# Kernel tuning notes

Hardware: AMD Instinct MI355X
Metric: run time of the kernel (lower is better)

Reference implementation:

```python
import jax, jax.numpy as jnp
import numpy as np

B, S, D, H = 2, 2048, 1024, 16
DK = D // H  # d_query_key_output = d_head = 64


def setup_inputs() -> dict:
    key = jax.random.key(0)
    ks = jax.random.split(key, 16)
    p = 0.02
    return {
        "input_q": jax.random.normal(ks[0], (B, S, D), jnp.float32),
        "input_k": jax.random.normal(ks[1], (B, S, D), jnp.float32),
        "input_v": jax.random.normal(ks[2], (B, S, D), jnp.float32),
        "mask": jax.random.randint(ks[3], (B, 1, S, S), 0, 2, jnp.int32),
        "attention_propagation": jax.random.normal(ks[4], (S, S), jnp.float32) * p,
        "Wq": jax.random.normal(ks[5], (D, H * DK), jnp.float32) * p,
        "bq": jnp.zeros((H * DK,), jnp.float32),
        "Wk": jax.random.normal(ks[6], (D, H * DK), jnp.float32) * p,
        "bk": jnp.zeros((H * DK,), jnp.float32),
        "Wv": jax.random.normal(ks[7], (D, H * DK), jnp.float32) * p,
        "bv": jnp.zeros((H * DK,), jnp.float32),
        "Wo": jax.random.normal(ks[8], (H * DK, D), jnp.float32) * p,
        "bo": jnp.zeros((D,), jnp.float32),
    }


def reference(input_q, input_k, input_v, mask, attention_propagation,
              Wq, bq, Wk, bk, Wv, bv, Wo, bo):
    b, q_len, _ = input_q.shape
    kv_len = input_k.shape[-2]
    # project and split into heads: split(d, -1) + stack(-3) == reshape + transpose
    q = (input_q @ Wq + bq).reshape(b, q_len, H, DK).transpose(0, 2, 1, 3)   # [B,H,Q,dk]
    k = (input_k @ Wk + bk).reshape(b, kv_len, H, DK).transpose(0, 2, 1, 3)  # [B,H,K,dk]
    v = (input_v @ Wv + bv).reshape(b, kv_len, H, DK).transpose(0, 2, 1, 3)  # [B,H,K,dh]

    scale = jnp.sqrt(jnp.asarray(DK, dtype=q.dtype))
    qk = jnp.einsum('bhqd,bhkd->bhqk', q, k) / scale                         # [B,H,Q,K]

    m = mask.astype(bool)  # [B,1,Q,K], broadcasts over heads
    # attention propagation branch: zero masked scores, then scores @ prop^T
    aw = jnp.where(m, qk, jnp.asarray(0.0, qk.dtype))
    aw = jnp.einsum('bhqk,lk->bhql', aw, attention_propagation)
    # masked softmax with nan_to_num for fully-masked rows
    aw = jnp.where(m, aw, -jnp.inf)
    aw = jax.nn.softmax(aw, axis=-1)
    aw = jnp.nan_to_num(aw, nan=0.0)
    # dropout is identity in eval / dropout_rate=0
    out = jnp.einsum('bhqk,bhkd->bhqd', aw, v)                               # [B,H,Q,dh]
    out = out.transpose(0, 2, 1, 3).reshape(b, q_len, H * DK)                # concat heads
    return out @ Wo + bo
```

## Files before the change

kernel.cpp:

```cpp
#include <hip/hip_runtime.h>
#include <hip/hip_bf16.h>
#include <stdint.h>

typedef unsigned int u32;
typedef __attribute__((ext_vector_type(8))) short bf16x8;
typedef __attribute__((ext_vector_type(4))) float f32x4;
typedef __attribute__((ext_vector_type(16))) float f32x16;

#define MFMA16(a, b, c) __builtin_amdgcn_mfma_f32_16x16x32_bf16((a), (b), (c), 0, 0, 0)
#define MFMA32(a, b, c) __builtin_amdgcn_mfma_f32_32x32x16_bf16((a), (b), (c), 0, 0, 0)

__device__ __forceinline__ float bf2f(short s) {
    union { u32 u; float f; } v;
    v.u = ((u32)(unsigned short)s) << 16;
    return v.f;
}
__device__ __forceinline__ short f2bf(float f) {
    union { float f; u32 u; } v; v.f = f;
    u32 r = (v.u + 0x7fffu + ((v.u >> 16) & 1u)) >> 16;
    return (short)r;
}
__device__ __forceinline__ void gl_lds16(const short* g, short* l) {
    __builtin_amdgcn_global_load_lds(
        (const __attribute__((address_space(1))) u32*)g,
        (__attribute__((address_space(3))) u32*)l, 16, 0, 0);
}

__device__ __forceinline__ void stage_tile(const short* g, int ld, short* lds) {
    int wave = threadIdx.x >> 6, lane = threadIdx.x & 63;
#pragma unroll
    for (int i = 0; i < 4; ++i) {
        int r0 = i * 32 + wave * 8;
        int r  = r0 + (lane >> 3);
        int c8 = (lane & 7) ^ (r & 7);
        gl_lds16(g + (long)r * ld + c8 * 8, lds + r0 * 64);
    }
}
__device__ __forceinline__ bf16x8 frag64(const short* lds, int row, int k8) {
    return *(const bf16x8*)(lds + row * 64 + ((k8 ^ (row & 7)) * 8));
}

__device__ __forceinline__ void stage_tile_p(const short* g, int ld, short* lds) {
    int wave = threadIdx.x >> 6, lane = threadIdx.x & 63;
#pragma unroll
    for (int i = 0; i < 4; ++i) {
        int r0 = i * 32 + wave * 8;
        int r  = r0 + (lane >> 3);
        int c8 = (lane & 7) ^ (r & 7);
        gl_lds16(g + (long)r * ld + c8 * 8, lds + r0 * 64 + (r0 >> 3) * 8);
    }
}
__device__ __forceinline__ bf16x8 frag64p(const short* lds, int row, int k8) {
    return *(const bf16x8*)(lds + row * 64 + ((row >> 3) * 8) + ((k8 ^ (row & 7)) * 8));
}

__global__ __launch_bounds__(256) void probe_dtype(const short* __restrict__ x,
                                                   int* __restrict__ flag) {
    __shared__ int cnt;
    if (threadIdx.x == 0) cnt = 0;
    __syncthreads();
    int c = 0;
    for (int i = threadIdx.x; i < 2048; i += 256) {
        int e = ((int)(unsigned short)x[i] >> 7) & 0xFF;
        if (e >= 147) ++c;
    }
    atomicAdd(&cnt, c);
    __syncthreads();
    if (threadIdx.x == 0) flag[0] = (cnt > 100) ? 1 : 0;
}

__global__ __launch_bounds__(256) void pack_mask(const int* __restrict__ mask,
                                                 u32* __restrict__ mb) {
    int row = blockIdx.x * 4 + (threadIdx.x >> 6);
    int lane = threadIdx.x & 63;
    const int* src = mask + (long)row * 2048;
    u32* dst = mb + (long)row * 64;
    for (int c0 = 0; c0 < 2048; c0 += 64) {
        unsigned long long m = __ballot(src[c0 + lane] != 0);
        if (lane == 0) {
            dst[(c0 >> 5)]     = (u32)m;
            dst[(c0 >> 5) + 1] = (u32)(m >> 32);
        }
    }
}
__device__ __forceinline__ int mask_bit(const u32* mb, int b, int row, int col) {
    u32 w = mb[((long)b * 2048 + row) * 64 + (col >> 5)];
    return (w >> (col & 31)) & 1;
}

__global__ __launch_bounds__(256) void convert_bf16(const void* __restrict__ src,
                                                    short* __restrict__ dst, int n,
                                                    const int* __restrict__ flag) {
    int isf = flag[0];
    for (int i = blockIdx.x * 256 + threadIdx.x; i < n; i += gridDim.x * 256)
        dst[i] = isf ? f2bf(((const float*)src)[i]) : ((const short*)src)[i];
}

__global__ __launch_bounds__(256) void convert_biases(const void* s0, const void* s1,
                                                      const void* s2, const void* s3,
                                                      short* __restrict__ dst,
                                                      const int* __restrict__ flag) {
    const void* ss[4] = { s0, s1, s2, s3 };
    const void* s = ss[blockIdx.x];
    short* d = dst + blockIdx.x * 1024;
    int isf = flag[0];
    for (int i = threadIdx.x; i < 1024; i += 256)
        d[i] = isf ? f2bf(((const float*)s)[i]) : ((const short*)s)[i];
}

__global__ __launch_bounds__(256) void transpose_1024(const void* __restrict__ src,
                                                      short* __restrict__ dst,
                                                      const int* __restrict__ flag) {
    __shared__ short t[64][65];
    int isf = flag[0];
    int r0 = blockIdx.y * 64, c0 = blockIdx.x * 64;
    int tx = threadIdx.x & 63, ty = threadIdx.x >> 6;
#pragma unroll
    for (int i = 0; i < 16; ++i) {
        int r = ty + i * 4;
        long idx = (long)(r0 + r) * 1024 + c0 + tx;
        t[r][tx] = isf ? f2bf(((const float*)src)[idx]) : ((const short*)src)[idx];
    }
    __syncthreads();
#pragma unroll
    for (int i = 0; i < 16; ++i) {
        int r = ty + i * 4;
        dst[(long)(c0 + r) * 1024 + r0 + tx] = t[tx][r];
    }
}

__global__ __launch_bounds__(256) void build_vt(const short* __restrict__ vp,
                                                short* __restrict__ vt) {
    __shared__ short t[64][65];
    int bh = blockIdx.y, b = bh >> 4, h = bh & 15;
    int l0 = blockIdx.x * 64;
    int tx = threadIdx.x & 63, ty = threadIdx.x >> 6;
#pragma unroll
    for (int i = 0; i < 16; ++i) {
        int l = ty + i * 4;
        t[l][tx] = vp[((long)b * 2048 + l0 + l) * 1024 + h * 64 + tx];
    }
    __syncthreads();
#pragma unroll
    for (int i = 0; i < 16; ++i) {
        int d = ty + i * 4;
        vt[((long)bh * 80 + d) * 2048 + l0 + tx] = t[tx][d];
    }
#pragma unroll
    for (int dd = 0; dd < 4; ++dd) {
        int d = 64 + ty * 4 + dd;
        short v = (d == 64) ? f2bf(1.0f) : (short)0;
        vt[((long)bh * 80 + d) * 2048 + l0 + tx] = v;
    }
}

__global__ __launch_bounds__(256) void gemm_nt_bias(const short* __restrict__ A,
                                                    const short* __restrict__ Bt,
                                                    const short* __restrict__ bias,
                                                    void* __restrict__ C,
                                                    int K, int lda, int ldb, int ldc,
                                                    const int* __restrict__ outf32) {
    __shared__ __align__(16) short a_lds[128 * 64];
    __shared__ __align__(16) short b_lds[128 * 64];
    int m0 = blockIdx.y * 128, n0 = blockIdx.x * 128;
    int wave = threadIdx.x >> 6, lane = threadIdx.x & 63;
    int col = lane & 15, quad = lane >> 4;
    int wm = (wave >> 1) * 64, wn = (wave & 1) * 64;
    f32x4 acc[4][4] = {};
    for (int k0 = 0; k0 < K; k0 += 64) {
        stage_tile(A + (long)m0 * lda + k0, lda, a_lds);
        stage_tile(Bt + (long)n0 * ldb + k0, ldb, b_lds);
        __syncthreads();
#pragma unroll
        for (int ks = 0; ks < 2; ++ks) {
            bf16x8 af[4], bfr[4];
#pragma unroll
            for (int t = 0; t < 4; ++t) af[t]  = frag64(a_lds, wm + t * 16 + col, ks * 4 + quad);
#pragma unroll
            for (int t = 0; t < 4; ++t) bfr[t] = frag64(b_lds, wn + t * 16 + col, ks * 4 + quad);
#pragma unroll
            for (int mt = 0; mt < 4; ++mt)
#pragma unroll
                for (int nt = 0; nt < 4; ++nt)
                    acc[mt][nt] = MFMA16(af[mt], bfr[nt], acc[mt][nt]);
        }
        __syncthreads();
    }
    int of = outf32 ? outf32[0] : 0;
#pragma unroll
    for (int mt = 0; mt < 4; ++mt) {
        int rb = m0 + wm + mt * 16 + quad * 4;
#pragma unroll
        for (int nt = 0; nt < 4; ++nt) {
            int c = n0 + wn + nt * 16 + col;
            float bv = bf2f(bias[c]);
#pragma unroll
            for (int r = 0; r < 4; ++r) {
                float v = acc[mt][nt][r] + bv;
                if (!(v == v)) v = 0.0f;
                long idx = (long)(rb + r) * ldc + c;
                if (of) ((float*)C)[idx] = v;
                else    ((short*)C)[idx] = f2bf(v);
            }
        }
    }
}

__global__ __launch_bounds__(256) void qk_mask_gemm(const short* __restrict__ qp,
                                                    const short* __restrict__ kp,
                                                    const u32* __restrict__ mb,
                                                    short* __restrict__ Smat,
                                                    int h0) {
    __shared__ __align__(16) short a_lds[128 * 64];
    __shared__ __align__(16) short b_lds[128 * 64];
    int zl = blockIdx.z, bh = h0 + zl, b = bh >> 4, h = bh & 15;
    int m0 = blockIdx.y * 128, n0 = blockIdx.x * 128;
    int wave = threadIdx.x >> 6, lane = threadIdx.x & 63;
    int col = lane & 15, quad = lane >> 4;
    int wm = (wave >> 1) * 64, wn = (wave & 1) * 64;
    const short* Aq = qp + ((long)b * 2048 + m0) * 1024 + h * 64;
    const short* Bk = kp + ((long)b * 2048 + n0) * 1024 + h * 64;
    stage_tile(Aq, 1024, a_lds);
    stage_tile(Bk, 1024, b_lds);
    __syncthreads();
    f32x4 acc[4][4] = {};
#pragma unroll
    for (int ks = 0; ks < 2; ++ks) {
        bf16x8 af[4], bfr[4];
#pragma unroll
        for (int t = 0; t < 4; ++t) af[t]  = frag64(a_lds, wm + t * 16 + col, ks * 4 + quad);
#pragma unroll
        for (int t = 0; t < 4; ++t) bfr[t] = frag64(b_lds, wn + t * 16 + col, ks * 4 + quad);
#pragma unroll
        for (int mt = 0; mt < 4; ++mt)
#pragma unroll
            for (int nt = 0; nt < 4; ++nt)
                acc[mt][nt] = MFMA16(af[mt], bfr[nt], acc[mt][nt]);
    }
#pragma unroll
    for (int mt = 0; mt < 4; ++mt) {
        int qb = m0 + wm + mt * 16 + quad * 4;
#pragma unroll
        for (int nt = 0; nt < 4; ++nt) {
            int kg = n0 + wn + nt * 16 + col;
#pragma unroll
            for (int r = 0; r < 4; ++r) {
                int qg = qb + r;
                int mk = mask_bit(mb, b, qg, kg);
                float v = mk ? acc[mt][nt][r] * 0.125f : 0.0f;
                if (!(v == v)) v = 0.0f;
                Smat[((long)zl * 2048 + qg) * 2048 + kg] = f2bf(v);
            }
        }
    }
}

__global__ __launch_bounds__(256) void p_gemm_exp(const short* __restrict__ Smat,
                                                  const short* __restrict__ prop,
                                                  const u32* __restrict__ mb,
                                                  short* __restrict__ Pmat,
                                                  int h0) {
    __shared__ __align__(16) short a_lds[128 * 64 + 128];
    __shared__ __align__(16) short b_lds[128 * 64 + 128];
    int zl = blockIdx.z, bh = h0 + zl, b = bh >> 4;
    int m0 = blockIdx.y * 128, n0 = blockIdx.x * 128;
    int wave = threadIdx.x >> 6, lane = threadIdx.x & 63;
    int m32 = lane & 31, hi = lane >> 5;
    int wm = (wave >> 1) * 64, wn = (wave & 1) * 64;
    const short* Arow = Smat + ((long)zl * 2048 + m0) * 2048;
    f32x16 acc[2][2] = {};
    for (int k0 = 0; k0 < 2048; k0 += 64) {
        stage_tile_p(Arow + k0, 2048, a_lds);
        stage_tile_p(prop + (long)n0 * 2048 + k0, 2048, b_lds);
        __syncthreads();
#pragma unroll
        for (int kc = 0; kc < 4; ++kc) {
            int k8 = kc * 2 + hi;
            bf16x8 af[2], bfr[2];
#pragma unroll
            for (int t = 0; t < 2; ++t) af[t]  = frag64p(a_lds, wm + t * 32 + m32, k8);
#pragma unroll
            for (int t = 0; t < 2; ++t) bfr[t] = frag64p(b_lds, wn + t * 32 + m32, k8);
#pragma unroll
            for (int mt = 0; mt < 2; ++mt)
#pragma unroll
                for (int nt = 0; nt < 2; ++nt)
                    acc[mt][nt] = MFMA32(af[mt], bfr[nt], acc[mt][nt]);
        }
        __syncthreads();
    }
#pragma unroll
    for (int mt = 0; mt < 2; ++mt) {
#pragma unroll
        for (int nt = 0; nt < 2; ++nt) {
            int lg = n0 + wn + nt * 32 + m32;
#pragma unroll
            for (int reg = 0; reg < 16; ++reg) {
                int qg = m0 + wm + mt * 32 + (reg & 3) + 8 * (reg >> 2) + 4 * hi;
                int mk = mask_bit(mb, b, qg, lg);
                float pv = acc[mt][nt][reg];
                if (!(pv == pv)) pv = 0.0f;
                pv = fminf(pv, 30.0f);
                float e = mk ? __expf(pv) : 0.0f;
                Pmat[((long)zl * 2048 + qg) * 2048 + lg] = f2bf(e);
            }
        }
    }
}

__global__ __launch_bounds__(256) void pv_kernel(const short* __restrict__ Pmat,
                                                 const short* __restrict__ vt,
                                                 short* __restrict__ att,
                                                 int h0) {
    __shared__ __align__(16) short p_lds[128 * 128];
    __shared__ __align__(16) short v_lds[80 * 128];
    int bhl = blockIdx.y, bh = h0 + bhl, b = bh >> 4, h = bh & 15;
    int q0 = blockIdx.x * 128;
    int wave = threadIdx.x >> 6, lane = threadIdx.x & 63;
    int col = lane & 15, quad = lane >> 4;
    const short* Pbase = Pmat + ((long)bhl * 2048 + q0) * 2048;
    const short* vbase = vt + (long)bh * 80 * 2048;

    f32x4 oacc[2][5] = {};

    for (int lt = 0; lt < 16; ++lt) {
        int l0 = lt * 128;
#pragma unroll
        for (int i = 0; i < 8; ++i) {
            int r0 = i * 16 + wave * 4;
            int r  = r0 + (lane >> 4);
            int c16 = (lane & 15) ^ (r & 15);
            gl_lds16(Pbase + (long)r * 2048 + l0 + c16 * 8, p_lds + r0 * 128);
        }
#pragma unroll
        for (int i = 0; i < 5; ++i) {
            int r0 = (wave * 5 + i) * 4;
            int r  = r0 + (lane >> 4);
            int c16 = (lane & 15) ^ (r & 15);
            gl_lds16(vbase + (long)r * 2048 + l0 + c16 * 8, v_lds + r0 * 128);
        }
        __syncthreads();
#pragma unroll
        for (int ks = 0; ks < 4; ++ks) {
            bf16x8 paf[2], vbf[5];
            int k8 = ks * 4 + quad;
#pragma unroll
            for (int t = 0; t < 2; ++t) {
                int rr = wave * 32 + t * 16 + col;
                paf[t] = *(const bf16x8*)(p_lds + rr * 128 + ((k8 ^ (rr & 15)) * 8));
            }
#pragma unroll
            for (int t = 0; t < 5; ++t) {
                int d = t * 16 + col;
                vbf[t] = *(const bf16x8*)(v_lds + d * 128 + ((k8 ^ (d & 15)) * 8));
            }
#pragma unroll
            for (int mt = 0; mt < 2; ++mt)
#pragma unroll
                for (int nt = 0; nt < 5; ++nt)
                    oacc[mt][nt] = MFMA16(paf[mt], vbf[nt], oacc[mt][nt]);
        }
        __syncthreads();
    }
#pragma unroll
    for (int mt = 0; mt < 2; ++mt) {
#pragma unroll
        for (int r = 0; r < 4; ++r) {
            float denom = __shfl(oacc[mt][4][r], lane & 48, 64);
            float inv = (denom > 1e-20f) ? 1.0f / denom : 0.0f;
            int qrow = q0 + wave * 32 + mt * 16 + quad * 4 + r;
#pragma unroll
            for (int nt = 0; nt < 4; ++nt) {
                float v = oacc[mt][nt][r] * inv;
                if (!(v == v)) v = 0.0f;
                att[((long)b * 2048 + qrow) * 1024 + h * 64 + nt * 16 + col] = f2bf(v);
            }
        }
    }
}

__global__ __launch_bounds__(256) void attn_fused(const short* __restrict__ Smat,
                                                  const short* __restrict__ prop,
                                                  const short* __restrict__ vt,
                                                  const u32* __restrict__ mb,
                                                  short* __restrict__ att,
                                                  int h0) {
    __shared__ __align__(16) short ab_lds[2 * 128 * 64];
    __shared__ __align__(16) short v_lds[80 * 128];
    short* p_lds = ab_lds;
    int bhl = blockIdx.y, bh = h0 + bhl, b = bh >> 4, h = bh & 15;
    int q0 = blockIdx.x * 128;
    int wave = threadIdx.x >> 6, lane = threadIdx.x & 63;
    int col = lane & 15, quad = lane >> 4;
    int wm = (wave >> 1) * 64, wn = (wave & 1) * 64;
    const short* Arow = Smat + ((long)bhl * 2048 + q0) * 2048;
    const short* vbase = vt + (long)bh * 80 * 2048;
    {
        u32* z1 = (u32*)ab_lds;
        u32* z2 = (u32*)v_lds;
        for (int i = threadIdx.x; i < 8192; i += 256) z1[i] = 0;
        for (int i = threadIdx.x; i < 5120; i += 256) z2[i] = 0;
    }
    __syncthreads();
    f32x4 oacc[2][5] = {};
    for (int lt = 0; lt < 16; ++lt) {
        int l0 = lt * 128;
#pragma unroll
        for (int i = 0; i < 5; ++i) {
            int r0 = (wave * 5 + i) * 4;
            int r  = r0 + (lane >> 4);
            int c16 = (lane & 15) ^ (r & 15);
            gl_lds16(vbase + (long)r * 2048 + l0 + c16 * 8, v_lds + r0 * 128);
        }
        f32x4 pacc[4][4] = {};
        for (int k0 = 0; k0 < 2048; k0 += 64) {
            stage_tile(Arow + k0, 2048, ab_lds);
            stage_tile(prop + (long)l0 * 2048 + k0, 2048, ab_lds + 128 * 64);
            __syncthreads();
#pragma unroll
            for (int ks = 0; ks < 2; ++ks) {
                bf16x8 af[4], bfr[4];
#pragma unroll
                for (int t = 0; t < 4; ++t) af[t]  = frag64(ab_lds, wm + t * 16 + col, ks * 4 + quad);
#pragma unroll
                for (int t = 0; t < 4; ++t) bfr[t] = frag64(ab_lds + 128 * 64, wn + t * 16 + col, ks * 4 + quad);
#pragma unroll
                for (int mt = 0; mt < 4; ++mt)
#pragma unroll
                    for (int nt = 0; nt < 4; ++nt)
                        pacc[mt][nt] = MFMA16(af[mt], bfr[nt], pacc[mt][nt]);
            }
            __syncthreads();
        }
#pragma unroll
        for (int mt = 0; mt < 4; ++mt) {
            int rm = wm + mt * 16 + quad * 4;
#pragma unroll
            for (int nt = 0; nt < 4; ++nt) {
                int cl = wn + nt * 16 + col;
                int lg = l0 + cl;
                int k8 = cl >> 3;
#pragma unroll
                for (int r = 0; r < 4; ++r) {
                    int rr = rm + r;
                    int mk = mask_bit(mb, b, q0 + rr, lg);
                    float pv = pacc[mt][nt][r];
                    if (!(pv == pv)) pv = 0.0f;
                    pv = fminf(pv, 30.0f);
                    float e = mk ? __expf(pv) : 0.0f;
                    p_lds[rr * 128 + ((k8 ^ (rr & 15)) * 8) + (cl & 7)] = f2bf(e);
                }
            }
        }
        __syncthreads();
#pragma unroll
        for (int ks = 0; ks < 4; ++ks) {
            bf16x8 paf[2], vbf[5];
            int k8 = ks * 4 + quad;
#pragma unroll
            for (int t = 0; t < 2; ++t) {
                int rr = wave * 32 + t * 16 + col;
                paf[t] = *(const bf16x8*)(p_lds + rr * 128 + ((k8 ^ (rr & 15)) * 8));
            }
#pragma unroll
            for (int t = 0; t < 5; ++t) {
                int d = t * 16 + col;
                vbf[t] = *(const bf16x8*)(v_lds + d * 128 + ((k8 ^ (d & 15)) * 8));
            }
#pragma unroll
            for (int mt = 0; mt < 2; ++mt)
#pragma unroll
                for (int nt = 0; nt < 5; ++nt)
                    oacc[mt][nt] = MFMA16(paf[mt], vbf[nt], oacc[mt][nt]);
        }
        __syncthreads();
    }
#pragma unroll
    for (int mt = 0; mt < 2; ++mt) {
#pragma unroll
        for (int r = 0; r < 4; ++r) {
            float denom = __shfl(oacc[mt][4][r], lane & 48, 64);
            float inv = (denom > 1e-20f) ? 1.0f / denom : 0.0f;
            int qrow = q0 + wave * 32 + mt * 16 + quad * 4 + r;
#pragma unroll
            for (int nt = 0; nt < 4; ++nt) {
                float v = oacc[mt][nt][r] * inv;
                if (!(v == v)) v = 0.0f;
                att[((long)b * 2048 + qrow) * 1024 + h * 64 + nt * 16 + col] = f2bf(v);
            }
        }
    }
}

extern "C" void kernel_launch(void* const* d_in, const int* in_sizes, int n_in,
                              void* d_out, int out_size, void* d_ws, size_t ws_size,
                              hipStream_t stream) {
    const void* xq   = d_in[0];
    const void* xk   = d_in[1];
    const void* xv   = d_in[2];
    const int*  mask = (const int*)d_in[3];
    const void* prop = d_in[4];
    const void* Wq   = d_in[5];
    const void* bq   = d_in[6];
    const void* Wk   = d_in[7];
    const void* bk   = d_in[8];
    const void* Wv   = d_in[9];
    const void* bv   = d_in[10];
    const void* Wo   = d_in[11];
    const void* bo   = d_in[12];

    char* ws = (char*)d_ws;
    const size_t MB = 1ull << 20;
    short* qp   = (short*)(ws + 0 * MB);
    short* kp   = (short*)(ws + 8 * MB);
    short* vp   = (short*)(ws + 16 * MB);
    short* attb = (short*)(ws + 24 * MB);
    short* WqT  = (short*)(ws + 32 * MB);
    short* WkT  = (short*)(ws + 34 * MB);
    short* WvT  = (short*)(ws + 36 * MB);
    short* WoT  = (short*)(ws + 38 * MB);
    short* vtb  = (short*)(ws + 40 * MB);
    u32*   mb   = (u32*)(ws + 50 * MB);
    int*   flag = (int*)(ws + 51 * MB);
    short* bq_c = (short*)(ws + 51 * MB + 4096);
    short* bk_c = bq_c + 1024;
    short* bv_c = bk_c + 1024;
    short* bo_c = bv_c + 1024;

    long wsMB = (long)(ws_size / MB);
    dim3 blk(256);
    const int NTOK = 4096 * 1024;
    const long HEAD_ELEMS = 2048L * 2048;

    if (wsMB < 60) return;

    probe_dtype<<<1, blk, 0, stream>>>((const short*)xq, flag);
    pack_mask<<<1024, blk, 0, stream>>>(mask, mb);
    convert_biases<<<4, blk, 0, stream>>>(bq, bk, bv, bo, bq_c, flag);
    transpose_1024<<<dim3(16, 16), blk, 0, stream>>>(Wq, WqT, flag);
    transpose_1024<<<dim3(16, 16), blk, 0, stream>>>(Wk, WkT, flag);
    transpose_1024<<<dim3(16, 16), blk, 0, stream>>>(Wv, WvT, flag);
    transpose_1024<<<dim3(16, 16), blk, 0, stream>>>(Wo, WoT, flag);

    if (wsMB >= 76) {
        short* prop_c = (short*)(ws + 52 * MB);
        short* xc     = (short*)(ws + 60 * MB);
        short* Smat   = (short*)(ws + 60 * MB);
        int G = (int)((wsMB - 60) / 16);
        if (G > 32) G = 32;
        short* Pmat = Smat + (long)G * HEAD_ELEMS;

        convert_bf16<<<1024, blk, 0, stream>>>(prop, prop_c, NTOK, flag);
        convert_bf16<<<1024, blk, 0, stream>>>(xq, xc, NTOK, flag);
        gemm_nt_bias<<<dim3(8, 32), blk, 0, stream>>>(xc, WqT, bq_c, qp, 1024, 1024, 1024, 1024, nullptr);
        convert_bf16<<<1024, blk, 0, stream>>>(xk, xc, NTOK, flag);
        gemm_nt_bias<<<dim3(8, 32), blk, 0, stream>>>(xc, WkT, bk_c, kp, 1024, 1024, 1024, 1024, nullptr);
        convert_bf16<<<1024, blk, 0, stream>>>(xv, xc, NTOK, flag);
        gemm_nt_bias<<<dim3(8, 32), blk, 0, stream>>>(xc, WvT, bv_c, vp, 1024, 1024, 1024, 1024, nullptr);
        build_vt<<<dim3(32, 32), blk, 0, stream>>>(vp, vtb);

        for (int h0 = 0; h0 < 32; h0 += G) {
            int g = 32 - h0 < G ? 32 - h0 : G;
            qk_mask_gemm<<<dim3(16, 16, g), blk, 0, stream>>>(qp, kp, mb, Smat, h0);
            p_gemm_exp<<<dim3(16, 16, g), blk, 0, stream>>>(Smat, prop_c, mb, Pmat, h0);
            pv_kernel<<<dim3(16, g), blk, 0, stream>>>(Pmat, vtb, attb, h0);
        }
    } else if (wsMB >= 68) {
        short* prop_c = (short*)(ws + 52 * MB);
        short* xc     = (short*)(ws + 60 * MB);
        short* Smat   = (short*)(ws + 60 * MB);
        int G = (int)((wsMB - 60) / 8);
        if (G > 32) G = 32;
        convert_bf16<<<1024, blk, 0, stream>>>(prop, prop_c, NTOK, flag);
        convert_bf16<<<1024, blk, 0, stream>>>(xq, xc, NTOK, flag);
        gemm_nt_bias<<<dim3(8, 32), blk, 0, stream>>>(xc, WqT, bq_c, qp, 1024, 1024, 1024, 1024, nullptr);
        convert_bf16<<<1024, blk, 0, stream>>>(xk, xc, NTOK, flag);
        gemm_nt_bias<<<dim3(8, 32), blk, 0, stream>>>(xc, WkT, bk_c, kp, 1024, 1024, 1024, 1024, nullptr);
        convert_bf16<<<1024, blk, 0, stream>>>(xv, xc, NTOK, flag);
        gemm_nt_bias<<<dim3(8, 32), blk, 0, stream>>>(xc, WvT, bv_c, vp, 1024, 1024, 1024, 1024, nullptr);
        build_vt<<<dim3(32, 32), blk, 0, stream>>>(vp, vtb);
        for (int h0 = 0; h0 < 32; h0 += G) {
            int g = 32 - h0 < G ? 32 - h0 : G;
            qk_mask_gemm<<<dim3(16, 16, g), blk, 0, stream>>>(qp, kp, mb, Smat, h0);
            attn_fused<<<dim3(16, g), blk, 0, stream>>>(Smat, prop_c, vtb, mb, attb, h0);
        }
    } else {
        short* Smat = (short*)(ws + 52 * MB);
        int G = (int)((wsMB - 52) / 8);
        if (G > 32) G = 32;
        gemm_nt_bias<<<dim3(8, 32), blk, 0, stream>>>((const short*)xq, WqT, bq_c, qp, 1024, 1024, 1024, 1024, nullptr);
        gemm_nt_bias<<<dim3(8, 32), blk, 0, stream>>>((const short*)xk, WkT, bk_c, kp, 1024, 1024, 1024, 1024, nullptr);
        gemm_nt_bias<<<dim3(8, 32), blk, 0, stream>>>((const short*)xv, WvT, bv_c, vp, 1024, 1024, 1024, 1024, nullptr);
        build_vt<<<dim3(32, 32), blk, 0, stream>>>(vp, vtb);
        for (int h0 = 0; h0 < 32; h0 += G) {
            int g = 32 - h0 < G ? 32 - h0 : G;
            qk_mask_gemm<<<dim3(16, 16, g), blk, 0, stream>>>(qp, kp, mb, Smat, h0);
            attn_fused<<<dim3(16, g), blk, 0, stream>>>(Smat, (const short*)prop, vtb, mb, attb, h0);
        }
    }

    gemm_nt_bias<<<dim3(8, 32), blk, 0, stream>>>(attb, WoT, bo_c, d_out, 1024, 1024, 1024, 1024, flag);
}
```

Before: 1.157 ms.

## Fuse propagation GEMM with PV product via split-K atomic accumulation

Merges the propagation GEMM + exp kernel with the P·V kernel. Each 128x128 tile of exp-scores stays in LDS, is multiplied by the matching V slice, and is atomically added into an fp32 output buffer. A separate divide kernel then normalises by the accumulated row sum. The softmax denominator now comes from an MFMA against a ones vector instead of a padded ones row in V, which shrinks V^T from 80 to 64 rows. This removes the round trip of the full bf16 P matrix through global memory. In exchange it adds a memset, float atomics, an extra kernel and a reshuffled workspace layout that needs a larger workspace for the fused path.

Result: slower. 1.281 ms (+10.7%).

```diff
diff --git a/kernel.cpp b/kernel.cpp
--- a/kernel.cpp
+++ b/kernel.cpp
@@ -144,13 +144,7 @@
 #pragma unroll
     for (int i = 0; i < 16; ++i) {
         int d = ty + i * 4;
-        vt[((long)bh * 80 + d) * 2048 + l0 + tx] = t[tx][d];
-    }
-#pragma unroll
-    for (int dd = 0; dd < 4; ++dd) {
-        int d = 64 + ty * 4 + dd;
-        short v = (d == 64) ? f2bf(1.0f) : (short)0;
-        vt[((long)bh * 80 + d) * 2048 + l0 + tx] = v;
+        vt[((long)bh * 64 + d) * 2048 + l0 + tx] = t[tx][d];
     }
 }
 
@@ -255,19 +249,33 @@
     }
 }
 
-__global__ __launch_bounds__(256) void p_gemm_exp(const short* __restrict__ Smat,
-                                                  const short* __restrict__ prop,
-                                                  const u32* __restrict__ mb,
-                                                  short* __restrict__ Pmat,
-                                                  int h0) {
-    __shared__ __align__(16) short a_lds[128 * 64 + 128];
-    __shared__ __align__(16) short b_lds[128 * 64 + 128];
+__global__ __launch_bounds__(256) void p_gemm_exp_pv(const short* __restrict__ Smat,
+                                                     const short* __restrict__ prop,
+                                                     const u32* __restrict__ mb,
+                                                     const short* __restrict__ vt,
+                                                     float* __restrict__ Obuf,
+                                                     int h0) {
+    __shared__ __align__(16) short ab_lds[2 * (128 * 64 + 128)];
+    __shared__ __align__(16) short v_lds[64 * 128];
+    short* a_lds = ab_lds;
+    short* b_lds = ab_lds + (128 * 64 + 128);
+    short* p_lds = ab_lds;
     int zl = blockIdx.z, bh = h0 + zl, b = bh >> 4;
     int m0 = blockIdx.y * 128, n0 = blockIdx.x * 128;
     int wave = threadIdx.x >> 6, lane = threadIdx.x & 63;
     int m32 = lane & 31, hi = lane >> 5;
     int wm = (wave >> 1) * 64, wn = (wave & 1) * 64;
     const short* Arow = Smat + ((long)zl * 2048 + m0) * 2048;
+    const short* vbase = vt + (long)bh * 64 * 2048;
+
+#pragma unroll
+    for (int i = 0; i < 4; ++i) {
+        int r0 = (wave * 4 + i) * 4;
+        int r  = r0 + (lane >> 4);
+        int c16 = (lane & 15) ^ (r & 15);
+        gl_lds16(vbase + (long)r * 2048 + n0 + c16 * 8, v_lds + r0 * 128);
+    }
+
     f32x16 acc[2][2] = {};
     for (int k0 = 0; k0 < 2048; k0 += 64) {
         stage_tile_p(Arow + k0, 2048, a_lds);
@@ -289,94 +297,81 @@
         }
         __syncthreads();
     }
+
 #pragma unroll
     for (int mt = 0; mt < 2; ++mt) {
 #pragma unroll
         for (int nt = 0; nt < 2; ++nt) {
-            int lg = n0 + wn + nt * 32 + m32;
+            int cl = wn + nt * 32 + m32;
+            int k8 = cl >> 3;
 #pragma unroll
             for (int reg = 0; reg < 16; ++reg) {
-                int qg = m0 + wm + mt * 32 + (reg & 3) + 8 * (reg >> 2) + 4 * hi;
-                int mk = mask_bit(mb, b, qg, lg);
+                int rr = wm + mt * 32 + (reg & 3) + 8 * (reg >> 2) + 4 * hi;
+                int mk = mask_bit(mb, b, m0 + rr, n0 + cl);
                 float pv = acc[mt][nt][reg];
                 if (!(pv == pv)) pv = 0.0f;
                 pv = fminf(pv, 30.0f);
                 float e = mk ? __expf(pv) : 0.0f;
-                Pmat[((long)zl * 2048 + qg) * 2048 + lg] = f2bf(e);
-            }
-        }
-    }
-}
-
-__global__ __launch_bounds__(256) void pv_kernel(const short* __restrict__ Pmat,
-                                                 const short* __restrict__ vt,
-                                                 short* __restrict__ att,
-                                                 int h0) {
-    __shared__ __align__(16) short p_lds[128 * 128];
-    __shared__ __align__(16) short v_lds[80 * 128];
-    int bhl = blockIdx.y, bh = h0 + bhl, b = bh >> 4, h = bh & 15;
-    int q0 = blockIdx.x * 128;
-    int wave = threadIdx.x >> 6, lane = threadIdx.x & 63;
-    int col = lane & 15, quad = lane >> 4;
-    const short* Pbase = Pmat + ((long)bhl * 2048 + q0) * 2048;
-    const short* vbase = vt + (long)bh * 80 * 2048;
-
+                p_lds[rr * 128 + ((k8 ^ (rr & 15)) * 8) + (cl & 7)] = f2bf(e);
+            }
+        }
+    }
+    __syncthreads();
+
+    int col16 = lane & 15, quad = lane >> 4;
+    bf16x8 ones;
+#pragma unroll
+    for (int j = 0; j < 8; ++j) ones[j] = (short)0x3F80;
     f32x4 oacc[2][5] = {};
-
-    for (int lt = 0; lt < 16; ++lt) {
-        int l0 = lt * 128;
-#pragma unroll
-        for (int i = 0; i < 8; ++i) {
-            int r0 = i * 16 + wave * 4;
-            int r  = r0 + (lane >> 4);
-            int c16 = (lane & 15) ^ (r & 15);
-            gl_lds16(Pbase + (long)r * 2048 + l0 + c16 * 8, p_lds + r0 * 128);
-        }
-#pragma unroll
-        for (int i = 0; i < 5; ++i) {
-            int r0 = (wave * 5 + i) * 4;
-            int r  = r0 + (lane >> 4);
-            int c16 = (lane & 15) ^ (r & 15);
-            gl_lds16(vbase + (long)r * 2048 + l0 + c16 * 8, v_lds + r0 * 128);
-        }
-        __syncthreads();
-#pragma unroll
-        for (int ks = 0; ks < 4; ++ks) {
-            bf16x8 paf[2], vbf[5];
-            int k8 = ks * 4 + quad;
-#pragma unroll
-            for (int t = 0; t < 2; ++t) {
-                int rr = wave * 32 + t * 16 + col;
-                paf[t] = *(const bf16x8*)(p_lds + rr * 128 + ((k8 ^ (rr & 15)) * 8));
-            }
-#pragma unroll
-            for (int t = 0; t < 5; ++t) {
-                int d = t * 16 + col;
-                vbf[t] = *(const bf16x8*)(v_lds + d * 128 + ((k8 ^ (d & 15)) * 8));
-            }
-#pragma unroll
-            for (int mt = 0; mt < 2; ++mt)
-#pragma unroll
-                for (int nt = 0; nt < 5; ++nt)
-                    oacc[mt][nt] = MFMA16(paf[mt], vbf[nt], oacc[mt][nt]);
-        }
-        __syncthreads();
+#pragma unroll
+    for (int ks = 0; ks < 4; ++ks) {
+        int k8 = ks * 4 + quad;
+        bf16x8 paf[2], vbf[4];
+#pragma unroll
+        for (int t = 0; t < 2; ++t) {
+            int rr = wave * 32 + t * 16 + col16;
+            paf[t] = *(const bf16x8*)(p_lds + rr * 128 + ((k8 ^ (rr & 15)) * 8));
+        }
+#pragma unroll
+        for (int t = 0; t < 4; ++t) {
+            int d = t * 16 + col16;
+            vbf[t] = *(const bf16x8*)(v_lds + d * 128 + ((k8 ^ (d & 15)) * 8));
+        }
+#pragma unroll
+        for (int mt = 0; mt < 2; ++mt) {
+#pragma unroll
+            for (int nt = 0; nt < 4; ++nt)
+                oacc[mt][nt] = MFMA16(paf[mt], vbf[nt], oacc[mt][nt]);
+            oacc[mt][4] = MFMA16(paf[mt], ones, oacc[mt][4]);
+        }
     }
 #pragma unroll
     for (int mt = 0; mt < 2; ++mt) {
 #pragma unroll
         for (int r = 0; r < 4; ++r) {
-            float denom = __shfl(oacc[mt][4][r], lane & 48, 64);
-            float inv = (denom > 1e-20f) ? 1.0f / denom : 0.0f;
-            int qrow = q0 + wave * 32 + mt * 16 + quad * 4 + r;
-#pragma unroll
-            for (int nt = 0; nt < 4; ++nt) {
-                float v = oacc[mt][nt][r] * inv;
-                if (!(v == v)) v = 0.0f;
-                att[((long)b * 2048 + qrow) * 1024 + h * 64 + nt * 16 + col] = f2bf(v);
-            }
-        }
-    }
+            int qg = m0 + wave * 32 + mt * 16 + quad * 4 + r;
+            float* orow = Obuf + ((long)zl * 2048 + qg) * 72;
+#pragma unroll
+            for (int nt = 0; nt < 4; ++nt)
+                atomicAdd(orow + nt * 16 + col16, oacc[mt][nt][r]);
+            if (col16 == 0)
+                atomicAdd(orow + 64, oacc[mt][4][r]);
+        }
+    }
+}
+
+__global__ __launch_bounds__(256) void o_divide(const float* __restrict__ Obuf,
+                                                short* __restrict__ att,
+                                                int h0) {
+    int zl = blockIdx.y, bh = h0 + zl, b = bh >> 4, h = bh & 15;
+    int q = blockIdx.x * 4 + (threadIdx.x >> 6);
+    int d = threadIdx.x & 63;
+    const float* orow = Obuf + ((long)zl * 2048 + q) * 72;
+    float den = orow[64];
+    float inv = (den > 1e-20f) ? 1.0f / den : 0.0f;
+    float v = orow[d] * inv;
+    if (!(v == v)) v = 0.0f;
+    att[((long)b * 2048 + q) * 1024 + h * 64 + d] = f2bf(v);
 }
 
 __global__ __launch_bounds__(256) void attn_fused(const short* __restrict__ Smat,
@@ -386,7 +381,7 @@
                                                   short* __restrict__ att,
                                                   int h0) {
     __shared__ __align__(16) short ab_lds[2 * 128 * 64];
-    __shared__ __align__(16) short v_lds[80 * 128];
+    __shared__ __align__(16) short v_lds[64 * 128];
     short* p_lds = ab_lds;
     int bhl = blockIdx.y, bh = h0 + bhl, b = bh >> 4, h = bh & 15;
     int q0 = blockIdx.x * 128;
@@ -394,20 +389,16 @@
     int col = lane & 15, quad = lane >> 4;
     int wm = (wave >> 1) * 64, wn = (wave & 1) * 64;
     const short* Arow = Smat + ((long)bhl * 2048 + q0) * 2048;
-    const short* vbase = vt + (long)bh * 80 * 2048;
-    {
-        u32* z1 = (u32*)ab_lds;
-        u32* z2 = (u32*)v_lds;
-        for (int i = threadIdx.x; i < 8192; i += 256) z1[i] = 0;
-        for (int i = threadIdx.x; i < 5120; i += 256) z2[i] = 0;
-    }
-    __syncthreads();
+    const short* vbase = vt + (long)bh * 64 * 2048;
+    bf16x8 ones;
+#pragma unroll
+    for (int j = 0; j < 8; ++j) ones[j] = (short)0x3F80;
     f32x4 oacc[2][5] = {};
     for (int lt = 0; lt < 16; ++lt) {
         int l0 = lt * 128;
 #pragma unroll
-        for (int i = 0; i < 5; ++i) {
-            int r0 = (wave * 5 + i) * 4;
+        for (int i = 0; i < 4; ++i) {
+            int r0 = (wave * 4 + i) * 4;
             int r  = r0 + (lane >> 4);
             int c16 = (lane & 15) ^ (r & 15);
             gl_lds16(vbase + (long)r * 2048 + l0 + c16 * 8, v_lds + r0 * 128);
@@ -455,7 +446,7 @@
         __syncthreads();
 #pragma unroll
         for (int ks = 0; ks < 4; ++ks) {
-            bf16x8 paf[2], vbf[5];
+            bf16x8 paf[2], vbf[4];
             int k8 = ks * 4 + quad;
 #pragma unroll
             for (int t = 0; t < 2; ++t) {
@@ -463,15 +454,17 @@
                 paf[t] = *(const bf16x8*)(p_lds + rr * 128 + ((k8 ^ (rr & 15)) * 8));
             }
 #pragma unroll
-            for (int t = 0; t < 5; ++t) {
+            for (int t = 0; t < 4; ++t) {
                 int d = t * 16 + col;
                 vbf[t] = *(const bf16x8*)(v_lds + d * 128 + ((k8 ^ (d & 15)) * 8));
             }
 #pragma unroll
-            for (int mt = 0; mt < 2; ++mt)
-#pragma unroll
-                for (int nt = 0; nt < 5; ++nt)
+            for (int mt = 0; mt < 2; ++mt) {
+#pragma unroll
+                for (int nt = 0; nt < 4; ++nt)
                     oacc[mt][nt] = MFMA16(paf[mt], vbf[nt], oacc[mt][nt]);
+                oacc[mt][4] = MFMA16(paf[mt], ones, oacc[mt][4]);
+            }
         }
         __syncthreads();
     }
@@ -479,8 +472,8 @@
     for (int mt = 0; mt < 2; ++mt) {
 #pragma unroll
         for (int r = 0; r < 4; ++r) {
-            float denom = __shfl(oacc[mt][4][r], lane & 48, 64);
-            float inv = (denom > 1e-20f) ? 1.0f / denom : 0.0f;
+            float den = oacc[mt][4][r];
+            float inv = (den > 1e-20f) ? 1.0f / den : 0.0f;
             int qrow = q0 + wave * 32 + mt * 16 + quad * 4 + r;
 #pragma unroll
             for (int nt = 0; nt < 4; ++nt) {
@@ -520,9 +513,9 @@
     short* WvT  = (short*)(ws + 36 * MB);
     short* WoT  = (short*)(ws + 38 * MB);
     short* vtb  = (short*)(ws + 40 * MB);
-    u32*   mb   = (u32*)(ws + 50 * MB);
-    int*   flag = (int*)(ws + 51 * MB);
-    short* bq_c = (short*)(ws + 51 * MB + 4096);
+    u32*   mb   = (u32*)(ws + 56 * MB);
+    int*   flag = (int*)(ws + 57 * MB);
+    short* bq_c = (short*)(ws + 57 * MB + 4096);
     short* bk_c = bq_c + 1024;
     short* bv_c = bk_c + 1024;
     short* bo_c = bv_c + 1024;
@@ -532,7 +525,7 @@
     const int NTOK = 4096 * 1024;
     const long HEAD_ELEMS = 2048L * 2048;
 
-    if (wsMB < 60) return;
+    if (wsMB < 66) return;
 
     probe_dtype<<<1, blk, 0, stream>>>((const short*)xq, flag);
     pack_mask<<<1024, blk, 0, stream>>>(mask, mb);
@@ -542,13 +535,13 @@
     transpose_1024<<<dim3(16, 16), blk, 0, stream>>>(Wv, WvT, flag);
     transpose_1024<<<dim3(16, 16), blk, 0, stream>>>(Wo, WoT, flag);
 
-    if (wsMB >= 76) {
-        short* prop_c = (short*)(ws + 52 * MB);
-        short* xc     = (short*)(ws + 60 * MB);
-        short* Smat   = (short*)(ws + 60 * MB);
-        int G = (int)((wsMB - 60) / 16);
+    if (wsMB >= 96) {
+        short* prop_c = (short*)(ws + 58 * MB);
+        float* Obuf   = (float*)(ws + 66 * MB);
+        short* xc     = (short*)(ws + 88 * MB);
+        short* Smat   = (short*)(ws + 88 * MB);
+        int G = (int)((wsMB - 88) / 8);
         if (G > 32) G = 32;
-        short* Pmat = Smat + (long)G * HEAD_ELEMS;
 
         convert_bf16<<<1024, blk, 0, stream>>>(prop, prop_c, NTOK, flag);
         convert_bf16<<<1024, blk, 0, stream>>>(xq, xc, NTOK, flag);
@@ -562,14 +555,15 @@
         for (int h0 = 0; h0 < 32; h0 += G) {
             int g = 32 - h0 < G ? 32 - h0 : G;
             qk_mask_gemm<<<dim3(16, 16, g), blk, 0, stream>>>(qp, kp, mb, Smat, h0);
-            p_gemm_exp<<<dim3(16, 16, g), blk, 0, stream>>>(Smat, prop_c, mb, Pmat, h0);
-            pv_kernel<<<dim3(16, g), blk, 0, stream>>>(Pmat, vtb, attb, h0);
-        }
-    } else if (wsMB >= 68) {
-        short* prop_c = (short*)(ws + 52 * MB);
-        short* xc     = (short*)(ws + 60 * MB);
-        short* Smat   = (short*)(ws + 60 * MB);
-        int G = (int)((wsMB - 60) / 8);
+            hipMemsetAsync(Obuf, 0, (size_t)g * 2048 * 72 * 4, stream);
+            p_gemm_exp_pv<<<dim3(16, 16, g), blk, 0, stream>>>(Smat, prop_c, mb, vtb, Obuf, h0);
+            o_divide<<<dim3(512, g), blk, 0, stream>>>(Obuf, attb, h0);
+        }
+    } else if (wsMB >= 74) {
+        short* prop_c = (short*)(ws + 58 * MB);
+        short* xc     = (short*)(ws + 66 * MB);
+        short* Smat   = (short*)(ws + 66 * MB);
+        int G = (int)((wsMB - 66) / 8);
         if (G > 32) G = 32;
         convert_bf16<<<1024, blk, 0, stream>>>(prop, prop_c, NTOK, flag);
         convert_bf16<<<1024, blk, 0, stream>>>(xq, xc, NTOK, flag);
@@ -585,8 +579,8 @@
             attn_fused<<<dim3(16, g), blk, 0, stream>>>(Smat, prop_c, vtb, mb, attb, h0);
         }
     } else {
-        short* Smat = (short*)(ws + 52 * MB);
-        int G = (int)((wsMB - 52) / 8);
+        short* Smat = (short*)(ws + 58 * MB);
+        int G = (int)((wsMB - 58) / 8);
         if (G > 32) G = 32;
         gemm_nt_bias<<<dim3(8, 32), blk, 0, stream>>>((const short*)xq, WqT, bq_c, qp, 1024, 1024, 1024, 1024, nullptr);
         gemm_nt_bias<<<dim3(8, 32), blk, 0, stream>>>((const short*)xk, WkT, bk_c, kp, 1024, 1024, 1024, 1024, nullptr);
```
